# Performance work log

Hardware: AMD Instinct MI355X
Metric: run time of the kernel (lower is better)

Reference implementation:

```python
import jax, jax.numpy as jnp
import numpy as np

W_CLS, W_BBOX, W_GIOU = 1.0, 5.0, 2.0
EPS = 1e-06


def _cxcywh_to_xyxy(box):
    cx, cy, w, h = box[..., 0], box[..., 1], box[..., 2], box[..., 3]
    return jnp.stack([cx - 0.5 * w, cy - 0.5 * h, cx + 0.5 * w, cy + 0.5 * h], axis=-1)


def _giou(b1, b2):
    # b1: [B, N, 4] xyxy, b2: [B, M, 4] xyxy -> giou [B, N, M]
    area1 = jnp.clip(b1[..., 2] - b1[..., 0], 0) * jnp.clip(b1[..., 3] - b1[..., 1], 0)  # [B,N]
    area2 = jnp.clip(b2[..., 2] - b2[..., 0], 0) * jnp.clip(b2[..., 3] - b2[..., 1], 0)  # [B,M]
    lt = jnp.maximum(b1[:, :, None, :2], b2[:, None, :, :2])  # [B,N,M,2]
    rb = jnp.minimum(b1[:, :, None, 2:], b2[:, None, :, 2:])
    wh = jnp.clip(rb - lt, 0)
    inter = wh[..., 0] * wh[..., 1]
    union = area1[:, :, None] + area2[:, None, :] - inter + EPS
    iou = inter / union
    lt_enc = jnp.minimum(b1[:, :, None, :2], b2[:, None, :, :2])
    rb_enc = jnp.maximum(b1[:, :, None, 2:], b2[:, None, :, 2:])
    wh_enc = jnp.clip(rb_enc - lt_enc, 0)
    enc = wh_enc[..., 0] * wh_enc[..., 1] + EPS
    return iou - (enc - union) / enc


def setup_inputs() -> dict:
    key = jax.random.key(0)
    k1, k2, k3, k4 = jax.random.split(key, 4)
    B, NQ, C, NT = 64, 900, 256, 128
    return {
        "pred_logits": jax.random.normal(k1, (B, NQ, C), dtype=jnp.float32),
        "pred_boxes": jax.random.uniform(k2, (B, NQ, 4), dtype=jnp.float32),
        "tgt_labels": jax.random.randint(k3, (B, NT), 0, C),
        "tgt_boxes": jax.random.uniform(k4, (B, NT, 4), dtype=jnp.float32),
    }


def reference(pred_logits, pred_boxes, tgt_labels, tgt_boxes):
    B, NQ, _ = pred_logits.shape
    NT = tgt_labels.shape[1]
    out_prob = jax.nn.softmax(pred_logits, axis=-1)  # [B,NQ,C]
    # gather class probs at target label ids: [B,NQ,NT]
    idx = jnp.broadcast_to(tgt_labels[:, None, :], (B, NQ, NT))
    cost_cls = -jnp.take_along_axis(out_prob, idx, axis=-1)
    # L1 cdist over cxcywh coords: [B,NQ,NT]
    cost_bbox = jnp.sum(jnp.abs(pred_boxes[:, :, None, :] - tgt_boxes[:, None, :, :]), axis=-1)
    giou = _giou(_cxcywh_to_xyxy(pred_boxes), _cxcywh_to_xyxy(tgt_boxes))
    cost_giou = -giou
    C = W_CLS * cost_cls + W_BBOX * cost_bbox + W_GIOU * cost_giou
    return C
```

## Files before the change

### kernel.cpp

```cpp
#include <hip/hip_runtime.h>

#define BB   64
#define NQ   900
#define NC   256
#define NT   128

#define RPW  4
#define RPB  16
#define NCHUNK 57

template<int CTRL>
__device__ __forceinline__ float dpp_add(float x) {
    int y = __builtin_amdgcn_update_dpp(0, __float_as_int(x), CTRL, 0xF, 0xF, true);
    return x + __int_as_float(y);
}

__global__ __launch_bounds__(256) void matcher_kernel(
    const float* __restrict__ logits,
    const float* __restrict__ pboxes,
    const int*   __restrict__ tlabels,
    const float* __restrict__ tboxes,
    float* __restrict__ out)
{
    constexpr float W_BBOX = 5.0f, W_GIOU = 2.0f, EPS = 1e-6f;

    __shared__ float sprob[RPB][NC];
    __shared__ float ssum[RPB];

    const int wave = threadIdx.x >> 6;
    const int lane = threadIdx.x & 63;
    const int g    = lane >> 4;
    const int j    = lane & 15;
    const int b    = blockIdx.y;
    const int q0   = blockIdx.x * RPB + wave * RPW;
    if (q0 >= NQ) return;
    const int wr0  = wave * RPW;

    const float* lrow = logits + ((size_t)b * NQ + q0 + g) * NC + j * 4;
    const float4 v0 = *reinterpret_cast<const float4*>(lrow);
    const float4 v1 = *reinterpret_cast<const float4*>(lrow + 64);
    const float4 v2 = *reinterpret_cast<const float4*>(lrow + 128);
    const float4 v3 = *reinterpret_cast<const float4*>(lrow + 192);

    float4 pb[RPW];
    #pragma unroll
    for (int r = 0; r < RPW; ++r)
        pb[r] = *reinterpret_cast<const float4*>(pboxes + ((size_t)b * NQ + q0 + r) * 4);

    const int t0 = lane * 2;
    const int2   lbl = *reinterpret_cast<const int2*>(tlabels + b * NT + t0);
    const float4 ta  = *reinterpret_cast<const float4*>(tboxes + ((size_t)b * NT + t0) * 4);
    const float4 tbv = *reinterpret_cast<const float4*>(tboxes + ((size_t)b * NT + t0 + 1) * 4);

    const float e0  = __expf(v0.x), e1  = __expf(v0.y), e2  = __expf(v0.z), e3  = __expf(v0.w);
    const float e4  = __expf(v1.x), e5  = __expf(v1.y), e6  = __expf(v1.z), e7  = __expf(v1.w);
    const float e8  = __expf(v2.x), e9  = __expf(v2.y), e10 = __expf(v2.z), e11 = __expf(v2.w);
    const float e12 = __expf(v3.x), e13 = __expf(v3.y), e14 = __expf(v3.z), e15 = __expf(v3.w);

    float* srow = &sprob[wr0 + g][j * 4];
    *reinterpret_cast<float4*>(srow)       = make_float4(e0,  e1,  e2,  e3);
    *reinterpret_cast<float4*>(srow + 64)  = make_float4(e4,  e5,  e6,  e7);
    *reinterpret_cast<float4*>(srow + 128) = make_float4(e8,  e9,  e10, e11);
    *reinterpret_cast<float4*>(srow + 192) = make_float4(e12, e13, e14, e15);

    float s = (((e0 + e1) + (e2 + e3)) + ((e4 + e5) + (e6 + e7)))
            + (((e8 + e9) + (e10 + e11)) + ((e12 + e13) + (e14 + e15)));
    s = dpp_add<0xB1>(s);
    s = dpp_add<0x4E>(s);
    s = dpp_add<0x141>(s);
    s = dpp_add<0x140>(s);
    if (j == 0) ssum[wr0 + g] = s;

    const float4 sums = *reinterpret_cast<const float4*>(&ssum[wr0]);
    const float inv[RPW] = { __builtin_amdgcn_rcpf(sums.x), __builtin_amdgcn_rcpf(sums.y),
                             __builtin_amdgcn_rcpf(sums.z), __builtin_amdgcn_rcpf(sums.w) };

    const float ax1 = ta.x - 0.5f * ta.z, ay1 = ta.y - 0.5f * ta.w;
    const float ax2 = ta.x + 0.5f * ta.z, ay2 = ta.y + 0.5f * ta.w;
    const float aarea = fmaxf(ax2 - ax1, 0.0f) * fmaxf(ay2 - ay1, 0.0f);
    const float bx1 = tbv.x - 0.5f * tbv.z, by1 = tbv.y - 0.5f * tbv.w;
    const float bx2 = tbv.x + 0.5f * tbv.z, by2 = tbv.y + 0.5f * tbv.w;
    const float barea = fmaxf(bx2 - bx1, 0.0f) * fmaxf(by2 - by1, 0.0f);

    #pragma unroll
    for (int r = 0; r < RPW; ++r) {
        const int wr = wr0 + r;
        const float p0 = sprob[wr][lbl.x] * inv[r];
        const float p1 = sprob[wr][lbl.y] * inv[r];

        const float px1 = pb[r].x - 0.5f * pb[r].z, py1 = pb[r].y - 0.5f * pb[r].w;
        const float px2 = pb[r].x + 0.5f * pb[r].z, py2 = pb[r].y + 0.5f * pb[r].w;
        const float parea = fmaxf(px2 - px1, 0.0f) * fmaxf(py2 - py1, 0.0f);

        const float l1a = fabsf(pb[r].x - ta.x) + fabsf(pb[r].y - ta.y)
                        + fabsf(pb[r].z - ta.z) + fabsf(pb[r].w - ta.w);
        const float ia  = fmaxf(fminf(px2, ax2) - fmaxf(px1, ax1), 0.0f)
                        * fmaxf(fminf(py2, ay2) - fmaxf(py1, ay1), 0.0f);
        const float ua  = parea + aarea - ia + EPS;
        const float ea  = fmaxf(fmaxf(px2, ax2) - fminf(px1, ax1), 0.0f)
                        * fmaxf(fmaxf(py2, ay2) - fminf(py1, ay1), 0.0f) + EPS;
        const float gioua = ia * __builtin_amdgcn_rcpf(ua)
                          - (ea - ua) * __builtin_amdgcn_rcpf(ea);
        const float c0 = -p0 + W_BBOX * l1a - W_GIOU * gioua;

        const float l1b = fabsf(pb[r].x - tbv.x) + fabsf(pb[r].y - tbv.y)
                        + fabsf(pb[r].z - tbv.z) + fabsf(pb[r].w - tbv.w);
        const float ib  = fmaxf(fminf(px2, bx2) - fmaxf(px1, bx1), 0.0f)
                        * fmaxf(fminf(py2, by2) - fmaxf(py1, by1), 0.0f);
        const float ub  = parea + barea - ib + EPS;
        const float eb  = fmaxf(fmaxf(px2, bx2) - fminf(px1, bx1), 0.0f)
                        * fmaxf(fmaxf(py2, by2) - fminf(py1, by1), 0.0f) + EPS;
        const float gioub = ib * __builtin_amdgcn_rcpf(ub)
                          - (eb - ub) * __builtin_amdgcn_rcpf(eb);
        const float c1 = -p1 + W_BBOX * l1b - W_GIOU * gioub;

        *reinterpret_cast<float2*>(out + ((size_t)b * NQ + q0 + r) * NT + t0) =
            make_float2(c0, c1);
    }
}

extern "C" void kernel_launch(void* const* d_in, const int* in_sizes, int n_in,
                              void* d_out, int out_size, void* d_ws, size_t ws_size,
                              hipStream_t stream) {
    const float* logits  = (const float*)d_in[0];
    const float* pboxes  = (const float*)d_in[1];
    const int*   tlabels = (const int*)d_in[2];
    const float* tboxes  = (const float*)d_in[3];
    float* out = (float*)d_out;

    dim3 grid(NCHUNK, BB);
    matcher_kernel<<<grid, 256, 0, stream>>>(logits, pboxes, tlabels, tboxes, out);
}
```

Baseline: 20.93 us.

## Process three row chunks per block with register double-buffered logits prefetch

Each block now loops over three 16-row chunks instead of one, cutting the grid from 57x64 to 19x64 blocks. While the current chunk is being computed, the logits for the next chunk are loaded into registers, which is meant to overlap memory latency with the softmax and GIoU math. Out-of-range rows are clamped and their stores skipped. The trade-off is fewer blocks in flight, which lowers occupancy for latency hiding, and higher register pressure. There is also no LDS barrier between iterations, though each wave only reads its own rows.

```diff
diff --git a/kernel.cpp b/kernel.cpp
--- a/kernel.cpp
+++ b/kernel.cpp
@@ -7,7 +7,8 @@
 
 #define RPW  4
 #define RPB  16
-#define NCHUNK 57
+#define CPB  3
+#define NBX  19
 
 template<int CTRL>
 __device__ __forceinline__ float dpp_add(float x) {
@@ -27,53 +28,18 @@
     __shared__ float sprob[RPB][NC];
     __shared__ float ssum[RPB];
 
-    const int wave = threadIdx.x >> 6;
-    const int lane = threadIdx.x & 63;
-    const int g    = lane >> 4;
-    const int j    = lane & 15;
-    const int b    = blockIdx.y;
-    const int q0   = blockIdx.x * RPB + wave * RPW;
-    if (q0 >= NQ) return;
-    const int wr0  = wave * RPW;
-
-    const float* lrow = logits + ((size_t)b * NQ + q0 + g) * NC + j * 4;
-    const float4 v0 = *reinterpret_cast<const float4*>(lrow);
-    const float4 v1 = *reinterpret_cast<const float4*>(lrow + 64);
-    const float4 v2 = *reinterpret_cast<const float4*>(lrow + 128);
-    const float4 v3 = *reinterpret_cast<const float4*>(lrow + 192);
-
-    float4 pb[RPW];
-    #pragma unroll
-    for (int r = 0; r < RPW; ++r)
-        pb[r] = *reinterpret_cast<const float4*>(pboxes + ((size_t)b * NQ + q0 + r) * 4);
+    const int wave   = threadIdx.x >> 6;
+    const int lane   = threadIdx.x & 63;
+    const int g      = lane >> 4;
+    const int j      = lane & 15;
+    const int b      = blockIdx.y;
+    const int chunk0 = blockIdx.x * CPB;
+    const int wr0    = wave * RPW;
 
     const int t0 = lane * 2;
     const int2   lbl = *reinterpret_cast<const int2*>(tlabels + b * NT + t0);
     const float4 ta  = *reinterpret_cast<const float4*>(tboxes + ((size_t)b * NT + t0) * 4);
     const float4 tbv = *reinterpret_cast<const float4*>(tboxes + ((size_t)b * NT + t0 + 1) * 4);
-
-    const float e0  = __expf(v0.x), e1  = __expf(v0.y), e2  = __expf(v0.z), e3  = __expf(v0.w);
-    const float e4  = __expf(v1.x), e5  = __expf(v1.y), e6  = __expf(v1.z), e7  = __expf(v1.w);
-    const float e8  = __expf(v2.x), e9  = __expf(v2.y), e10 = __expf(v2.z), e11 = __expf(v2.w);
-    const float e12 = __expf(v3.x), e13 = __expf(v3.y), e14 = __expf(v3.z), e15 = __expf(v3.w);
-
-    float* srow = &sprob[wr0 + g][j * 4];
-    *reinterpret_cast<float4*>(srow)       = make_float4(e0,  e1,  e2,  e3);
-    *reinterpret_cast<float4*>(srow + 64)  = make_float4(e4,  e5,  e6,  e7);
-    *reinterpret_cast<float4*>(srow + 128) = make_float4(e8,  e9,  e10, e11);
-    *reinterpret_cast<float4*>(srow + 192) = make_float4(e12, e13, e14, e15);
-
-    float s = (((e0 + e1) + (e2 + e3)) + ((e4 + e5) + (e6 + e7)))
-            + (((e8 + e9) + (e10 + e11)) + ((e12 + e13) + (e14 + e15)));
-    s = dpp_add<0xB1>(s);
-    s = dpp_add<0x4E>(s);
-    s = dpp_add<0x141>(s);
-    s = dpp_add<0x140>(s);
-    if (j == 0) ssum[wr0 + g] = s;
-
-    const float4 sums = *reinterpret_cast<const float4*>(&ssum[wr0]);
-    const float inv[RPW] = { __builtin_amdgcn_rcpf(sums.x), __builtin_amdgcn_rcpf(sums.y),
-                             __builtin_amdgcn_rcpf(sums.z), __builtin_amdgcn_rcpf(sums.w) };
 
     const float ax1 = ta.x - 0.5f * ta.z, ay1 = ta.y - 0.5f * ta.w;
     const float ax2 = ta.x + 0.5f * ta.z, ay2 = ta.y + 0.5f * ta.w;
@@ -82,40 +48,107 @@
     const float bx2 = tbv.x + 0.5f * tbv.z, by2 = tbv.y + 0.5f * tbv.w;
     const float barea = fmaxf(bx2 - bx1, 0.0f) * fmaxf(by2 - by1, 0.0f);
 
+    auto rowptr = [&](int p) {
+        int q = (chunk0 + p) * RPB + wr0 + g;
+        q = q < NQ - 1 ? q : NQ - 1;
+        return logits + ((size_t)b * NQ + q) * NC + j * 4;
+    };
+
+    float4 cur[4], nxt[4];
+    {
+        const float* lp = rowptr(0);
+        cur[0] = *reinterpret_cast<const float4*>(lp);
+        cur[1] = *reinterpret_cast<const float4*>(lp + 64);
+        cur[2] = *reinterpret_cast<const float4*>(lp + 128);
+        cur[3] = *reinterpret_cast<const float4*>(lp + 192);
+    }
+
     #pragma unroll
-    for (int r = 0; r < RPW; ++r) {
-        const int wr = wr0 + r;
-        const float p0 = sprob[wr][lbl.x] * inv[r];
-        const float p1 = sprob[wr][lbl.y] * inv[r];
+    for (int p = 0; p < CPB; ++p) {
+        const int q0 = (chunk0 + p) * RPB + wr0;
 
-        const float px1 = pb[r].x - 0.5f * pb[r].z, py1 = pb[r].y - 0.5f * pb[r].w;
-        const float px2 = pb[r].x + 0.5f * pb[r].z, py2 = pb[r].y + 0.5f * pb[r].w;
-        const float parea = fmaxf(px2 - px1, 0.0f) * fmaxf(py2 - py1, 0.0f);
+        float4 pb[RPW];
+        #pragma unroll
+        for (int r = 0; r < RPW; ++r) {
+            int q = q0 + r; q = q < NQ - 1 ? q : NQ - 1;
+            pb[r] = *reinterpret_cast<const float4*>(pboxes + ((size_t)b * NQ + q) * 4);
+        }
 
-        const float l1a = fabsf(pb[r].x - ta.x) + fabsf(pb[r].y - ta.y)
-                        + fabsf(pb[r].z - ta.z) + fabsf(pb[r].w - ta.w);
-        const float ia  = fmaxf(fminf(px2, ax2) - fmaxf(px1, ax1), 0.0f)
-                        * fmaxf(fminf(py2, ay2) - fmaxf(py1, ay1), 0.0f);
-        const float ua  = parea + aarea - ia + EPS;
-        const float ea  = fmaxf(fmaxf(px2, ax2) - fminf(px1, ax1), 0.0f)
-                        * fmaxf(fmaxf(py2, ay2) - fminf(py1, ay1), 0.0f) + EPS;
-        const float gioua = ia * __builtin_amdgcn_rcpf(ua)
-                          - (ea - ua) * __builtin_amdgcn_rcpf(ea);
-        const float c0 = -p0 + W_BBOX * l1a - W_GIOU * gioua;
+        if (p + 1 < CPB) {
+            const float* lp = rowptr(p + 1);
+            nxt[0] = *reinterpret_cast<const float4*>(lp);
+            nxt[1] = *reinterpret_cast<const float4*>(lp + 64);
+            nxt[2] = *reinterpret_cast<const float4*>(lp + 128);
+            nxt[3] = *reinterpret_cast<const float4*>(lp + 192);
+        }
 
-        const float l1b = fabsf(pb[r].x - tbv.x) + fabsf(pb[r].y - tbv.y)
-                        + fabsf(pb[r].z - tbv.z) + fabsf(pb[r].w - tbv.w);
-        const float ib  = fmaxf(fminf(px2, bx2) - fmaxf(px1, bx1), 0.0f)
-                        * fmaxf(fminf(py2, by2) - fmaxf(py1, by1), 0.0f);
-        const float ub  = parea + barea - ib + EPS;
-        const float eb  = fmaxf(fmaxf(px2, bx2) - fminf(px1, bx1), 0.0f)
-                        * fmaxf(fmaxf(py2, by2) - fminf(py1, by1), 0.0f) + EPS;
-        const float gioub = ib * __builtin_amdgcn_rcpf(ub)
-                          - (eb - ub) * __builtin_amdgcn_rcpf(eb);
-        const float c1 = -p1 + W_BBOX * l1b - W_GIOU * gioub;
+        const float e0  = __expf(cur[0].x), e1  = __expf(cur[0].y),
+                    e2  = __expf(cur[0].z), e3  = __expf(cur[0].w);
+        const float e4  = __expf(cur[1].x), e5  = __expf(cur[1].y),
+                    e6  = __expf(cur[1].z), e7  = __expf(cur[1].w);
+        const float e8  = __expf(cur[2].x), e9  = __expf(cur[2].y),
+                    e10 = __expf(cur[2].z), e11 = __expf(cur[2].w);
+        const float e12 = __expf(cur[3].x), e13 = __expf(cur[3].y),
+                    e14 = __expf(cur[3].z), e15 = __expf(cur[3].w);
 
-        *reinterpret_cast<float2*>(out + ((size_t)b * NQ + q0 + r) * NT + t0) =
-            make_float2(c0, c1);
+        float* srow = &sprob[wr0 + g][j * 4];
+        *reinterpret_cast<float4*>(srow)       = make_float4(e0,  e1,  e2,  e3);
+        *reinterpret_cast<float4*>(srow + 64)  = make_float4(e4,  e5,  e6,  e7);
+        *reinterpret_cast<float4*>(srow + 128) = make_float4(e8,  e9,  e10, e11);
+        *reinterpret_cast<float4*>(srow + 192) = make_float4(e12, e13, e14, e15);
+
+        float s = (((e0 + e1) + (e2 + e3)) + ((e4 + e5) + (e6 + e7)))
+                + (((e8 + e9) + (e10 + e11)) + ((e12 + e13) + (e14 + e15)));
+        s = dpp_add<0xB1>(s);
+        s = dpp_add<0x4E>(s);
+        s = dpp_add<0x141>(s);
+        s = dpp_add<0x140>(s);
+        if (j == 0) ssum[wr0 + g] = s;
+
+        const float4 sums = *reinterpret_cast<const float4*>(&ssum[wr0]);
+        const float inv[RPW] = {
+            __builtin_amdgcn_rcpf(sums.x), __builtin_amdgcn_rcpf(sums.y),
+            __builtin_amdgcn_rcpf(sums.z), __builtin_amdgcn_rcpf(sums.w) };
+
+        #pragma unroll
+        for (int r = 0; r < RPW; ++r) {
+            const int wr = wr0 + r;
+            const float p0 = sprob[wr][lbl.x] * inv[r];
+            const float p1 = sprob[wr][lbl.y] * inv[r];
+
+            const float px1 = pb[r].x - 0.5f * pb[r].z, py1 = pb[r].y - 0.5f * pb[r].w;
+            const float px2 = pb[r].x + 0.5f * pb[r].z, py2 = pb[r].y + 0.5f * pb[r].w;
+            const float parea = fmaxf(px2 - px1, 0.0f) * fmaxf(py2 - py1, 0.0f);
+
+            const float l1a = fabsf(pb[r].x - ta.x) + fabsf(pb[r].y - ta.y)
+                            + fabsf(pb[r].z - ta.z) + fabsf(pb[r].w - ta.w);
+            const float ia  = fmaxf(fminf(px2, ax2) - fmaxf(px1, ax1), 0.0f)
+                            * fmaxf(fminf(py2, ay2) - fmaxf(py1, ay1), 0.0f);
+            const float ua  = parea + aarea - ia + EPS;
+            const float ea  = fmaxf(fmaxf(px2, ax2) - fminf(px1, ax1), 0.0f)
+                            * fmaxf(fmaxf(py2, ay2) - fminf(py1, ay1), 0.0f) + EPS;
+            const float gioua = ia * __builtin_amdgcn_rcpf(ua)
+                              - (ea - ua) * __builtin_amdgcn_rcpf(ea);
+            const float c0 = -p0 + W_BBOX * l1a - W_GIOU * gioua;
+
+            const float l1b = fabsf(pb[r].x - tbv.x) + fabsf(pb[r].y - tbv.y)
+                            + fabsf(pb[r].z - tbv.z) + fabsf(pb[r].w - tbv.w);
+            const float ib  = fmaxf(fminf(px2, bx2) - fmaxf(px1, bx1), 0.0f)
+                            * fmaxf(fminf(py2, by2) - fmaxf(py1, by1), 0.0f);
+            const float ub  = parea + barea - ib + EPS;
+            const float eb  = fmaxf(fmaxf(px2, bx2) - fminf(px1, bx1), 0.0f)
+                            * fmaxf(fmaxf(py2, by2) - fminf(py1, by1), 0.0f) + EPS;
+            const float gioub = ib * __builtin_amdgcn_rcpf(ub)
+                              - (eb - ub) * __builtin_amdgcn_rcpf(eb);
+            const float c1 = -p1 + W_BBOX * l1b - W_GIOU * gioub;
+
+            if (q0 < NQ)
+                *reinterpret_cast<float2*>(out + ((size_t)b * NQ + q0 + r) * NT + t0) =
+                    make_float2(c0, c1);
+        }
+
+        #pragma unroll
+        for (int k = 0; k < 4; ++k) cur[k] = nxt[k];
     }
 }
 
@@ -128,6 +161,6 @@
     const float* tboxes  = (const float*)d_in[3];
     float* out = (float*)d_out;
 
-    dim3 grid(NCHUNK, BB);
+    dim3 grid(NBX, BB);
     matcher_kernel<<<grid, 256, 0, stream>>>(logits, pboxes, tlabels, tboxes, out);
 }
```

Result: slower. 22.08 us (+5.5%).

## Store raw logits to LDS, broadcast sums via readlane, nontemporal output stores

Applied to the files above, without the earlier changes.

Raw logits now go to shared memory and the gathered label entries are read early, so the gather no longer waits on the exp computation. The exp is recomputed only for the gathered values. Row sums are broadcast across the wave with readlane instead of going through LDS, which removes one shared-memory round trip. Logit row indices are clamped to stay in bounds, and output uses nontemporal stores to reduce cache pollution. The cost is eight extra exps per lane and readlane scalar traffic.

```diff
diff --git a/kernel.cpp b/kernel.cpp
--- a/kernel.cpp
+++ b/kernel.cpp
@@ -9,10 +9,16 @@
 #define RPB  16
 #define NCHUNK 57
 
+typedef float f32x2 __attribute__((ext_vector_type(2)));
+
 template<int CTRL>
 __device__ __forceinline__ float dpp_add(float x) {
     int y = __builtin_amdgcn_update_dpp(0, __float_as_int(x), CTRL, 0xF, 0xF, true);
     return x + __int_as_float(y);
+}
+
+__device__ __forceinline__ float lane_bcast(float x, int l) {
+    return __int_as_float(__builtin_amdgcn_readlane(__float_as_int(x), l));
 }
 
 __global__ __launch_bounds__(256) void matcher_kernel(
@@ -24,8 +30,7 @@
 {
     constexpr float W_BBOX = 5.0f, W_GIOU = 2.0f, EPS = 1e-6f;
 
-    __shared__ float sprob[RPB][NC];
-    __shared__ float ssum[RPB];
+    __shared__ __align__(16) float raw[RPB][NC];
 
     const int wave = threadIdx.x >> 6;
     const int lane = threadIdx.x & 63;
@@ -36,7 +41,8 @@
     if (q0 >= NQ) return;
     const int wr0  = wave * RPW;
 
-    const float* lrow = logits + ((size_t)b * NQ + q0 + g) * NC + j * 4;
+    int qg = q0 + g; qg = qg < NQ - 1 ? qg : NQ - 1;
+    const float* lrow = logits + ((size_t)b * NQ + qg) * NC + j * 4;
     const float4 v0 = *reinterpret_cast<const float4*>(lrow);
     const float4 v1 = *reinterpret_cast<const float4*>(lrow + 64);
     const float4 v2 = *reinterpret_cast<const float4*>(lrow + 128);
@@ -52,28 +58,33 @@
     const float4 ta  = *reinterpret_cast<const float4*>(tboxes + ((size_t)b * NT + t0) * 4);
     const float4 tbv = *reinterpret_cast<const float4*>(tboxes + ((size_t)b * NT + t0 + 1) * 4);
 
-    const float e0  = __expf(v0.x), e1  = __expf(v0.y), e2  = __expf(v0.z), e3  = __expf(v0.w);
-    const float e4  = __expf(v1.x), e5  = __expf(v1.y), e6  = __expf(v1.z), e7  = __expf(v1.w);
-    const float e8  = __expf(v2.x), e9  = __expf(v2.y), e10 = __expf(v2.z), e11 = __expf(v2.w);
-    const float e12 = __expf(v3.x), e13 = __expf(v3.y), e14 = __expf(v3.z), e15 = __expf(v3.w);
+    float* srow = &raw[wr0 + g][j * 4];
+    *reinterpret_cast<float4*>(srow)       = v0;
+    *reinterpret_cast<float4*>(srow + 64)  = v1;
+    *reinterpret_cast<float4*>(srow + 128) = v2;
+    *reinterpret_cast<float4*>(srow + 192) = v3;
 
-    float* srow = &sprob[wr0 + g][j * 4];
-    *reinterpret_cast<float4*>(srow)       = make_float4(e0,  e1,  e2,  e3);
-    *reinterpret_cast<float4*>(srow + 64)  = make_float4(e4,  e5,  e6,  e7);
-    *reinterpret_cast<float4*>(srow + 128) = make_float4(e8,  e9,  e10, e11);
-    *reinterpret_cast<float4*>(srow + 192) = make_float4(e12, e13, e14, e15);
+    float ga[RPW], gb[RPW];
+    #pragma unroll
+    for (int r = 0; r < RPW; ++r) {
+        ga[r] = raw[wr0 + r][lbl.x];
+        gb[r] = raw[wr0 + r][lbl.y];
+    }
 
-    float s = (((e0 + e1) + (e2 + e3)) + ((e4 + e5) + (e6 + e7)))
-            + (((e8 + e9) + (e10 + e11)) + ((e12 + e13) + (e14 + e15)));
+    float s = (((__expf(v0.x) + __expf(v0.y)) + (__expf(v0.z) + __expf(v0.w)))
+            +  ((__expf(v1.x) + __expf(v1.y)) + (__expf(v1.z) + __expf(v1.w))))
+            + (((__expf(v2.x) + __expf(v2.y)) + (__expf(v2.z) + __expf(v2.w)))
+            +  ((__expf(v3.x) + __expf(v3.y)) + (__expf(v3.z) + __expf(v3.w))));
     s = dpp_add<0xB1>(s);
     s = dpp_add<0x4E>(s);
     s = dpp_add<0x141>(s);
     s = dpp_add<0x140>(s);
-    if (j == 0) ssum[wr0 + g] = s;
 
-    const float4 sums = *reinterpret_cast<const float4*>(&ssum[wr0]);
-    const float inv[RPW] = { __builtin_amdgcn_rcpf(sums.x), __builtin_amdgcn_rcpf(sums.y),
-                             __builtin_amdgcn_rcpf(sums.z), __builtin_amdgcn_rcpf(sums.w) };
+    const float inv[RPW] = {
+        __builtin_amdgcn_rcpf(lane_bcast(s, 0)),
+        __builtin_amdgcn_rcpf(lane_bcast(s, 16)),
+        __builtin_amdgcn_rcpf(lane_bcast(s, 32)),
+        __builtin_amdgcn_rcpf(lane_bcast(s, 48)) };
 
     const float ax1 = ta.x - 0.5f * ta.z, ay1 = ta.y - 0.5f * ta.w;
     const float ax2 = ta.x + 0.5f * ta.z, ay2 = ta.y + 0.5f * ta.w;
@@ -84,9 +95,8 @@
 
     #pragma unroll
     for (int r = 0; r < RPW; ++r) {
-        const int wr = wr0 + r;
-        const float p0 = sprob[wr][lbl.x] * inv[r];
-        const float p1 = sprob[wr][lbl.y] * inv[r];
+        const float p0 = __expf(ga[r]) * inv[r];
+        const float p1 = __expf(gb[r]) * inv[r];
 
         const float px1 = pb[r].x - 0.5f * pb[r].z, py1 = pb[r].y - 0.5f * pb[r].w;
         const float px2 = pb[r].x + 0.5f * pb[r].z, py2 = pb[r].y + 0.5f * pb[r].w;
@@ -114,8 +124,9 @@
                           - (eb - ub) * __builtin_amdgcn_rcpf(eb);
         const float c1 = -p1 + W_BBOX * l1b - W_GIOU * gioub;
 
-        *reinterpret_cast<float2*>(out + ((size_t)b * NQ + q0 + r) * NT + t0) =
-            make_float2(c0, c1);
+        f32x2 cc; cc.x = c0; cc.y = c1;
+        __builtin_nontemporal_store(cc,
+            reinterpret_cast<f32x2*>(out + ((size_t)b * NQ + q0 + r) * NT + t0));
     }
 }
 
```

After: 20.99 us. Within noise of the previous version (+0.3%).
